# Kernel tuning notes

Hardware: AMD Instinct MI355X
Metric: run time of the kernel (lower is better)

## Reference

```python
import jax, jax.numpy as jnp
import numpy as np
from jax import lax


def _log_g(z):
    # log of g(x) = x + 0.5 if x >= 0 else sigmoid(x)
    return jnp.where(z >= 0, jnp.log(jax.nn.relu(z) + 0.5), -jax.nn.softplus(-z))


def setup_inputs() -> dict:
    key = jax.random.key(0)
    k1, k2, k3 = jax.random.split(key, 3)
    B, S, D, H = 8, 8192, 512, 256
    x = jax.random.normal(k1, (B, S, D), dtype=jnp.float32)
    h_prev = jax.random.normal(k2, (B, H), dtype=jnp.float32)
    # nn.Linear(D, 3H, bias=False) weight: [3H, D], scaled like torch default init
    W = jax.random.normal(k3, (3 * H, D), dtype=jnp.float32) * (1.0 / np.sqrt(D))
    return {"x": x, "h_prev": h_prev, "W": W}


def reference(x, h_prev, W):
    # x: [B,S,D], h_prev: [B,H], W: [3H,D]
    seq_len = x.shape[1]
    y = jnp.einsum("bsd,hd->bsh", x, W)              # [B,S,3H]
    f, i, h = jnp.split(y, 3, axis=-1)                # each [B,S,H]
    diff = jax.nn.softplus(-f) - jax.nn.softplus(-i)
    log_f = -jax.nn.softplus(diff)                    # log(sigmoid-normalized forget gate)
    log_i = -jax.nn.softplus(-diff)                   # log(input gate)
    log_h0 = _log_g(h_prev)                           # [B,H]
    log_tilde_h = _log_g(h)                           # [B,S,H]
    # parallel scan in log space: h_t = f_t * h_{t-1} + i_t * g(h_t~)
    a_star = jnp.concatenate(
        [jnp.zeros_like(log_h0)[:, None], jnp.cumsum(log_f, axis=1)], axis=1
    )                                                  # [B,S+1,H]
    log_vals = jnp.concatenate([log_h0[:, None], log_i + log_tilde_h], axis=1)  # [B,S+1,H]
    log_h = a_star + lax.cumlogsumexp(log_vals - a_star, axis=1)
    h_t = jnp.exp(log_h)                               # [B,S+1,H]
    return h_t[:, -seq_len:]                           # [B,S,H]
```

## Files before the change

kernel.cpp:

```cpp
#include <hip/hip_runtime.h>
#include <math.h>

#define BB 8
#define SS 8192
#define DD 512
#define HH 256
#define MM (BB * SS)
#define NN (3 * HH)
#define CC 64
#define LL 128

typedef unsigned short u16;
typedef __attribute__((ext_vector_type(8))) short short8;
typedef __attribute__((ext_vector_type(4))) float f32x4;

#define AS1(p) ((const __attribute__((address_space(1))) void*)(p))
#define AS3(p) ((__attribute__((address_space(3))) void*)(p))

__device__ __forceinline__ u16 f2bf(float f) {
    union { float f; unsigned u; } v; v.f = f;
    unsigned r = v.u + 0x7fffu + ((v.u >> 16) & 1u);
    return (u16)(r >> 16);
}

__device__ __forceinline__ float sp_fast(float z) {
    return (z > 15.0f) ? z : __logf(1.0f + __expf(z));
}

__global__ __launch_bounds__(256) void convert_x(const float4* __restrict__ x,
                                                 ushort4* __restrict__ xb, int n4) {
    int i = blockIdx.x * blockDim.x + threadIdx.x;
    const int stride = gridDim.x * blockDim.x;
    for (; i < n4; i += stride) {
        const float4 v = x[i];
        ushort4 o;
        o.x = f2bf(v.x); o.y = f2bf(v.y); o.z = f2bf(v.z); o.w = f2bf(v.w);
        xb[i] = o;
    }
}

__global__ __launch_bounds__(128) void convert_W(const float* __restrict__ W,
                                                 u16* __restrict__ Wr) {
    const int orow = blockIdx.x;
    const int hg = orow / 48, rem = orow % 48;
    const int g = rem >> 4, hl = rem & 15;
    const int irow = g * HH + hg * 16 + hl;
    const int t = threadIdx.x;
    const float4 v = *(const float4*)&W[(size_t)irow * DD + t * 4];
    ushort4 o;
    o.x = f2bf(v.x); o.y = f2bf(v.y); o.z = f2bf(v.z); o.w = f2bf(v.w);
    *(ushort4*)&Wr[(size_t)orow * DD + t * 4] = o;
}

__global__ __launch_bounds__(512) void gemm_gate_mfma(
    const u16* __restrict__ Wr,
    float* __restrict__ F_arr,
    void* xbuf)
{
    __shared__ __align__(16) u16 As[64 * 32];
    __shared__ __align__(16) u16 Bs[NN * 32];

    const u16* xb = (const u16*)xbuf;
    float* u_out = (float*)xbuf;

    const int tid = threadIdx.x;
    const int m0 = blockIdx.x * 64;
    const int w = tid >> 6;
    const int lane = tid & 63;
    const int l16 = lane & 15;
    const int quad = lane >> 4;

    f32x4 acc[4][6];
    #pragma unroll
    for (int a = 0; a < 4; ++a)
        #pragma unroll
        for (int b = 0; b < 6; ++b)
            #pragma unroll
            for (int e = 0; e < 4; ++e) acc[a][b][e] = 0.0f;

    for (int kit = 0; kit < DD / 32; ++kit) {
        const int k0 = kit * 32;
        __syncthreads();
        #pragma unroll
        for (int i = 0; i < 6; ++i) {
            const int idx = tid + 512 * i;
            const u16* g = Wr + ((size_t)(idx >> 2) * DD + k0 + (idx & 3) * 8);
            __builtin_amdgcn_global_load_lds(AS1(g), AS3(Bs + (size_t)idx * 8), 16, 0, 0);
        }
        if (tid < 256) {
            const int idx = tid;
            const u16* g = xb + ((size_t)(m0 + (idx >> 2)) * DD + k0 + (idx & 3) * 8);
            __builtin_amdgcn_global_load_lds(AS1(g), AS3(As + (size_t)idx * 8), 16, 0, 0);
        }
        __syncthreads();

        short8 a[4], b[6];
        #pragma unroll
        for (int mf = 0; mf < 4; ++mf)
            a[mf] = *(const short8*)&As[(mf * 16 + l16) * 32 + quad * 8];
        #pragma unroll
        for (int nf = 0; nf < 6; ++nf)
            b[nf] = *(const short8*)&Bs[(w * 96 + nf * 16 + l16) * 32 + quad * 8];
        #pragma unroll
        for (int mf = 0; mf < 4; ++mf)
            #pragma unroll
            for (int nf = 0; nf < 6; ++nf)
                acc[mf][nf] = __builtin_amdgcn_mfma_f32_16x16x32_bf16(
                    a[mf], b[nf], acc[mf][nf], 0, 0, 0);
    }

    #pragma unroll
    for (int mf = 0; mf < 4; ++mf) {
        #pragma unroll
        for (int hgl = 0; hgl < 2; ++hgl) {
            const int head = (2 * w + hgl) * 16 + l16;
            #pragma unroll
            for (int r = 0; r < 4; ++r) {
                const int m = m0 + mf * 16 + quad * 4 + r;
                const float fr = acc[mf][hgl * 3 + 0][r];
                const float ir = acc[mf][hgl * 3 + 1][r];
                const float hr = acc[mf][hgl * 3 + 2][r];
                const float diff = sp_fast(-fr) - sp_fast(-ir);
                const float F = __builtin_amdgcn_rcpf(1.0f + __expf(diff));
                const float I = 1.0f - F;
                const float G = (hr >= 0.0f) ? (hr + 0.5f)
                                             : __builtin_amdgcn_rcpf(1.0f + __expf(-hr));
                const size_t o = (size_t)m * HH + head;
                F_arr[o] = F;
                u_out[o] = I * G;
            }
        }
    }
}

__global__ __launch_bounds__(256) void scan_pass1(
    const float* __restrict__ F_arr, const float* __restrict__ u_arr,
    float* __restrict__ P_arr, float* __restrict__ U_arr) {
    const int bc = blockIdx.x;
    const int b = bc / CC;
    const int c = bc % CC;
    const int h = threadIdx.x;
    size_t base = ((size_t)(b * SS + c * LL)) * HH + h;
    float P = 1.0f, U = 0.0f;
    #pragma unroll 4
    for (int t = 0; t < LL; ++t) {
        const float F = F_arr[base];
        const float u = u_arr[base];
        U = F * U + u;
        P = P * F;
        base += HH;
    }
    const size_t o = ((size_t)c * BB + b) * HH + h;
    P_arr[o] = P;
    U_arr[o] = U;
}

__global__ __launch_bounds__(256) void scan_pass2(
    const float* __restrict__ h_prev, const float* __restrict__ P_arr,
    const float* __restrict__ U_arr, float* __restrict__ Hin) {
    const int b = blockIdx.x;
    const int h = threadIdx.x;
    const float z = h_prev[b * HH + h];
    float carry = (z >= 0.0f) ? (z + 0.5f) : __builtin_amdgcn_rcpf(1.0f + __expf(-z));
    for (int c = 0; c < CC; ++c) {
        const size_t o = ((size_t)c * BB + b) * HH + h;
        Hin[o] = carry;
        carry = P_arr[o] * carry + U_arr[o];
    }
}

__global__ __launch_bounds__(256) void scan_pass3(
    const float* __restrict__ F_arr, const float* __restrict__ Hin,
    float* __restrict__ out) {
    const int bc = blockIdx.x;
    const int b = bc / CC;
    const int c = bc % CC;
    const int h = threadIdx.x;
    float hv = Hin[((size_t)c * BB + b) * HH + h];
    size_t base = ((size_t)(b * SS + c * LL)) * HH + h;
    #pragma unroll 4
    for (int t = 0; t < LL; ++t) {
        const float F = F_arr[base];
        const float u = out[base];
        hv = F * hv + u;
        out[base] = hv;
        base += HH;
    }
}

extern "C" void kernel_launch(void* const* d_in, const int* in_sizes, int n_in,
                              void* d_out, int out_size, void* d_ws, size_t ws_size,
                              hipStream_t stream) {
    const float* x      = (const float*)d_in[0];
    const float* h_prev = (const float*)d_in[1];
    const float* W      = (const float*)d_in[2];

    float* F_arr = (float*)d_ws;
    float* P_arr = F_arr + (size_t)MM * HH;
    float* U_arr = P_arr + (size_t)CC * BB * HH;
    float* Hin   = U_arr + (size_t)CC * BB * HH;
    u16*   Wr    = (u16*)(Hin + (size_t)CC * BB * HH);

    convert_x<<<4096, 256, 0, stream>>>((const float4*)x, (ushort4*)d_out,
                                        (MM * DD) / 4);
    convert_W<<<NN, 128, 0, stream>>>(W, Wr);
    gemm_gate_mfma<<<MM / 64, 512, 0, stream>>>(Wr, F_arr, d_out);
    scan_pass1<<<BB * CC, HH, 0, stream>>>(F_arr, (const float*)d_out, P_arr, U_arr);
    scan_pass2<<<BB, HH, 0, stream>>>(h_prev, P_arr, U_arr, Hin);
    scan_pass3<<<BB * CC, HH, 0, stream>>>(F_arr, Hin, (float*)d_out);
}
```

Before: 387.9 us.

## Fuse x bf16 conversion into GEMM and double-buffer W tiles in LDS

Removes the separate convert_x pass: the GEMM now reads fp32 x directly, packs it to bf16 with round-to-nearest and stores it into a padded, double-buffered A tile in LDS. W is pre-packed into a tile-contiguous layout split into two N-halves, so each half is prefetched into LDS while the other is used by MFMA. The goal is to save a full read/write pass over x (about 128MB in, 64MB out) and to overlap loads with compute. In exchange the GEMM reads twice as many A bytes, rounding of x changes slightly, and the kernel uses more LDS per block, which may lower occupancy.

Measured after the change: 346.8 us. 1.12x faster.

```diff
diff --git a/kernel.cpp b/kernel.cpp
--- a/kernel.cpp
+++ b/kernel.cpp
@@ -6,7 +6,7 @@
 #define DD 512
 #define HH 256
 #define MM (BB * SS)
-#define NN (3 * HH)
+#define NN 768
 #define CC 64
 #define LL 128
 
@@ -17,51 +17,48 @@
 #define AS1(p) ((const __attribute__((address_space(1))) void*)(p))
 #define AS3(p) ((__attribute__((address_space(3))) void*)(p))
 
-__device__ __forceinline__ u16 f2bf(float f) {
+__device__ __forceinline__ u16 f2bf_rtne(float f) {
     union { float f; unsigned u; } v; v.f = f;
     unsigned r = v.u + 0x7fffu + ((v.u >> 16) & 1u);
     return (u16)(r >> 16);
 }
+__device__ __forceinline__ unsigned pack2_rtn(float a, float b) {
+    union { float f; unsigned u; } x, y; x.f = a; y.f = b;
+    return ((x.u + 0x8000u) >> 16) | ((y.u + 0x8000u) & 0xffff0000u);
+}
 
 __device__ __forceinline__ float sp_fast(float z) {
     return (z > 15.0f) ? z : __logf(1.0f + __expf(z));
 }
 
-__global__ __launch_bounds__(256) void convert_x(const float4* __restrict__ x,
-                                                 ushort4* __restrict__ xb, int n4) {
-    int i = blockIdx.x * blockDim.x + threadIdx.x;
-    const int stride = gridDim.x * blockDim.x;
-    for (; i < n4; i += stride) {
-        const float4 v = x[i];
-        ushort4 o;
-        o.x = f2bf(v.x); o.y = f2bf(v.y); o.z = f2bf(v.z); o.w = f2bf(v.w);
-        xb[i] = o;
-    }
-}
-
-__global__ __launch_bounds__(128) void convert_W(const float* __restrict__ W,
+__global__ __launch_bounds__(256) void convert_W(const float* __restrict__ W,
                                                  u16* __restrict__ Wr) {
-    const int orow = blockIdx.x;
-    const int hg = orow / 48, rem = orow % 48;
-    const int g = rem >> 4, hl = rem & 15;
-    const int irow = g * HH + hg * 16 + hl;
-    const int t = threadIdx.x;
-    const float4 v = *(const float4*)&W[(size_t)irow * DD + t * 4];
-    ushort4 o;
-    o.x = f2bf(v.x); o.y = f2bf(v.y); o.z = f2bf(v.z); o.w = f2bf(v.w);
-    *(ushort4*)&Wr[(size_t)orow * DD + t * 4] = o;
+    const int chunk = blockIdx.x * 256 + threadIdx.x;
+    const int kh = chunk / 1536;
+    const int rem = chunk % 1536;
+    const int cl = rem >> 2, qq = rem & 3;
+    const int kc = kh >> 1, half = kh & 1;
+    const int c = half * 384 + cl;
+    const int hg = c / 48, r48 = c % 48;
+    const int g = r48 >> 4, hl = r48 & 15;
+    const int wrow = g * HH + hg * 16 + hl;
+    const int k0 = kc * 32 + qq * 8;
+    const float4 v0 = *(const float4*)&W[(size_t)wrow * DD + k0];
+    const float4 v1 = *(const float4*)&W[(size_t)wrow * DD + k0 + 4];
+    u16 o[8];
+    o[0]=f2bf_rtne(v0.x); o[1]=f2bf_rtne(v0.y); o[2]=f2bf_rtne(v0.z); o[3]=f2bf_rtne(v0.w);
+    o[4]=f2bf_rtne(v1.x); o[5]=f2bf_rtne(v1.y); o[6]=f2bf_rtne(v1.z); o[7]=f2bf_rtne(v1.w);
+    *(uint4*)&Wr[(size_t)chunk * 8] = *(const uint4*)o;
 }
 
 __global__ __launch_bounds__(512) void gemm_gate_mfma(
+    const float* __restrict__ x,
     const u16* __restrict__ Wr,
     float* __restrict__ F_arr,
-    void* xbuf)
+    float* __restrict__ u_out)
 {
-    __shared__ __align__(16) u16 As[64 * 32];
-    __shared__ __align__(16) u16 Bs[NN * 32];
-
-    const u16* xb = (const u16*)xbuf;
-    float* u_out = (float*)xbuf;
+    __shared__ __align__(16) u16 Bs[2][12288];
+    __shared__ __align__(16) u16 As[2][64 * 40];
 
     const int tid = threadIdx.x;
     const int m0 = blockIdx.x * 64;
@@ -70,6 +67,9 @@
     const int l16 = lane & 15;
     const int quad = lane >> 4;
 
+    const int arow = tid >> 3;
+    const int aqi = tid & 7;
+
     f32x4 acc[4][6];
     #pragma unroll
     for (int a = 0; a < 4; ++a)
@@ -78,48 +78,90 @@
             #pragma unroll
             for (int e = 0; e < 4; ++e) acc[a][b][e] = 0.0f;
 
-    for (int kit = 0; kit < DD / 32; ++kit) {
-        const int k0 = kit * 32;
-        __syncthreads();
-        #pragma unroll
-        for (int i = 0; i < 6; ++i) {
-            const int idx = tid + 512 * i;
-            const u16* g = Wr + ((size_t)(idx >> 2) * DD + k0 + (idx & 3) * 8);
-            __builtin_amdgcn_global_load_lds(AS1(g), AS3(Bs + (size_t)idx * 8), 16, 0, 0);
-        }
-        if (tid < 256) {
-            const int idx = tid;
-            const u16* g = xb + ((size_t)(m0 + (idx >> 2)) * DD + k0 + (idx & 3) * 8);
-            __builtin_amdgcn_global_load_lds(AS1(g), AS3(As + (size_t)idx * 8), 16, 0, 0);
-        }
-        __syncthreads();
-
-        short8 a[4], b[6];
+    #pragma unroll
+    for (int i = 0; i < 3; ++i) {
+        const int idx = i * 512 + tid;
+        __builtin_amdgcn_global_load_lds(AS1(Wr + (size_t)idx * 8),
+                                         AS3(&Bs[0][idx * 8]), 16, 0, 0);
+    }
+    {
+        const float4 v = *(const float4*)&x[(size_t)(m0 + arow) * DD + aqi * 4];
+        *(uint2*)&As[0][arow * 40 + aqi * 4] =
+            make_uint2(pack2_rtn(v.x, v.y), pack2_rtn(v.z, v.w));
+    }
+    float4 a_reg = *(const float4*)&x[(size_t)(m0 + arow) * DD + 32 + aqi * 4];
+    __syncthreads();
+
+    for (int kc = 0; kc < 16; ++kc) {
+        {
+            const size_t base = ((size_t)(kc * 2 + 1)) * 12288;
+            #pragma unroll
+            for (int i = 0; i < 3; ++i) {
+                const int idx = i * 512 + tid;
+                __builtin_amdgcn_global_load_lds(AS1(Wr + base + (size_t)idx * 8),
+                                                 AS3(&Bs[1][idx * 8]), 16, 0, 0);
+            }
+        }
+        short8 afr[4];
         #pragma unroll
         for (int mf = 0; mf < 4; ++mf)
-            a[mf] = *(const short8*)&As[(mf * 16 + l16) * 32 + quad * 8];
+            afr[mf] = *(const short8*)&As[kc & 1][(mf * 16 + l16) * 40 + quad * 8];
+
+        {
+            short8 bfr[3];
+            #pragma unroll
+            for (int jn = 0; jn < 3; ++jn)
+                bfr[jn] = *(const short8*)&Bs[0][((w * 3 + jn) * 16 + l16) * 32 + quad * 8];
+            #pragma unroll
+            for (int mf = 0; mf < 4; ++mf)
+                #pragma unroll
+                for (int jn = 0; jn < 3; ++jn)
+                    acc[mf][jn] = __builtin_amdgcn_mfma_f32_16x16x32_bf16(
+                        afr[mf], bfr[jn], acc[mf][jn], 0, 0, 0);
+        }
+        *(uint2*)&As[(kc + 1) & 1][arow * 40 + aqi * 4] =
+            make_uint2(pack2_rtn(a_reg.x, a_reg.y), pack2_rtn(a_reg.z, a_reg.w));
+        {
+            const int knext = (kc + 2 < 16) ? (kc + 2) : 15;
+            a_reg = *(const float4*)&x[(size_t)(m0 + arow) * DD + knext * 32 + aqi * 4];
+        }
+        __syncthreads();
+
+        if (kc < 15) {
+            const size_t base = ((size_t)((kc + 1) * 2)) * 12288;
+            #pragma unroll
+            for (int i = 0; i < 3; ++i) {
+                const int idx = i * 512 + tid;
+                __builtin_amdgcn_global_load_lds(AS1(Wr + base + (size_t)idx * 8),
+                                                 AS3(&Bs[0][idx * 8]), 16, 0, 0);
+            }
+        }
+        {
+            short8 bfr[3];
+            #pragma unroll
+            for (int jn = 0; jn < 3; ++jn)
+                bfr[jn] = *(const short8*)&Bs[1][((w * 3 + jn) * 16 + l16) * 32 + quad * 8];
+            #pragma unroll
+            for (int mf = 0; mf < 4; ++mf)
+                #pragma unroll
+                for (int jn = 0; jn < 3; ++jn)
+                    acc[mf][3 + jn] = __builtin_amdgcn_mfma_f32_16x16x32_bf16(
+                        afr[mf], bfr[jn], acc[mf][3 + jn], 0, 0, 0);
+        }
+        __syncthreads();
+    }
+
+    #pragma unroll
+    for (int half = 0; half < 2; ++half) {
+        const int head = (half * 8 + w) * 16 + l16;
         #pragma unroll
-        for (int nf = 0; nf < 6; ++nf)
-            b[nf] = *(const short8*)&Bs[(w * 96 + nf * 16 + l16) * 32 + quad * 8];
-        #pragma unroll
-        for (int mf = 0; mf < 4; ++mf)
-            #pragma unroll
-            for (int nf = 0; nf < 6; ++nf)
-                acc[mf][nf] = __builtin_amdgcn_mfma_f32_16x16x32_bf16(
-                    a[mf], b[nf], acc[mf][nf], 0, 0, 0);
-    }
-
-    #pragma unroll
-    for (int mf = 0; mf < 4; ++mf) {
-        #pragma unroll
-        for (int hgl = 0; hgl < 2; ++hgl) {
-            const int head = (2 * w + hgl) * 16 + l16;
+        for (int mf = 0; mf < 4; ++mf) {
             #pragma unroll
             for (int r = 0; r < 4; ++r) {
                 const int m = m0 + mf * 16 + quad * 4 + r;
-                const float fr = acc[mf][hgl * 3 + 0][r];
-                const float ir = acc[mf][hgl * 3 + 1][r];
-                const float hr = acc[mf][hgl * 3 + 2][r];
+                const float fr = acc[mf][half * 3 + 0][r];
+                const float ir = acc[mf][half * 3 + 1][r];
+                const float hr = acc[mf][half * 3 + 2][r];
                 const float diff = sp_fast(-fr) - sp_fast(-ir);
                 const float F = __builtin_amdgcn_rcpf(1.0f + __expf(diff));
                 const float I = 1.0f - F;
@@ -201,10 +243,8 @@
     float* Hin   = U_arr + (size_t)CC * BB * HH;
     u16*   Wr    = (u16*)(Hin + (size_t)CC * BB * HH);
 
-    convert_x<<<4096, 256, 0, stream>>>((const float4*)x, (ushort4*)d_out,
-                                        (MM * DD) / 4);
-    convert_W<<<NN, 128, 0, stream>>>(W, Wr);
-    gemm_gate_mfma<<<MM / 64, 512, 0, stream>>>(Wr, F_arr, d_out);
+    convert_W<<<192, 256, 0, stream>>>(W, Wr);
+    gemm_gate_mfma<<<MM / 64, 512, 0, stream>>>(x, Wr, F_arr, (float*)d_out);
     scan_pass1<<<BB * CC, HH, 0, stream>>>(F_arr, (const float*)d_out, P_arr, U_arr);
     scan_pass2<<<BB, HH, 0, stream>>>(h_prev, P_arr, U_arr, Hin);
     scan_pass3<<<BB * CC, HH, 0, stream>>>(F_arr, Hin, (float*)d_out);
```

## Fuse x conversion and chunk scan into GEMM epilogue, pack F/u as bf16

Applied to the files above, without the earlier changes.

Drops the separate x-to-bf16 kernel: the GEMM now reads fp32 x directly into registers, converts it, and feeds MFMA from registers with software prefetch instead of LDS staging. The GEMM epilogue also computes per-64-row chunk products and sums via wave shuffles, which removes the first scan pass. F and u are stored as a packed bf16 pair to halve intermediate traffic. The cost is lower precision in the recurrence inputs (round-to-nearest bf16 for F, u, P and U), which may hurt accuracy over long chains, and each wave now loads its A and B operands from global memory without LDS sharing.

Result: slower. 429.8 us (+10.8%).

```diff
diff --git a/kernel.cpp b/kernel.cpp
--- a/kernel.cpp
+++ b/kernel.cpp
@@ -6,37 +6,28 @@
 #define DD 512
 #define HH 256
 #define MM (BB * SS)
-#define NN (3 * HH)
 #define CC 64
 #define LL 128
 
 typedef unsigned short u16;
+typedef unsigned int u32;
 typedef __attribute__((ext_vector_type(8))) short short8;
 typedef __attribute__((ext_vector_type(4))) float f32x4;
 
-#define AS1(p) ((const __attribute__((address_space(1))) void*)(p))
-#define AS3(p) ((__attribute__((address_space(3))) void*)(p))
-
-__device__ __forceinline__ u16 f2bf(float f) {
+__device__ __forceinline__ u16 f2bf_rtne(float f) {
     union { float f; unsigned u; } v; v.f = f;
     unsigned r = v.u + 0x7fffu + ((v.u >> 16) & 1u);
     return (u16)(r >> 16);
 }
+__device__ __forceinline__ u32 pack2_rtn(float a, float b) {
+    union { float f; unsigned u; } x, y; x.f = a; y.f = b;
+    return ((x.u + 0x8000u) >> 16) | ((y.u + 0x8000u) & 0xffff0000u);
+}
+__device__ __forceinline__ float bf_lo(u32 w) { return __uint_as_float(w << 16); }
+__device__ __forceinline__ float bf_hi(u32 w) { return __uint_as_float(w & 0xffff0000u); }
 
 __device__ __forceinline__ float sp_fast(float z) {
     return (z > 15.0f) ? z : __logf(1.0f + __expf(z));
-}
-
-__global__ __launch_bounds__(256) void convert_x(const float4* __restrict__ x,
-                                                 ushort4* __restrict__ xb, int n4) {
-    int i = blockIdx.x * blockDim.x + threadIdx.x;
-    const int stride = gridDim.x * blockDim.x;
-    for (; i < n4; i += stride) {
-        const float4 v = x[i];
-        ushort4 o;
-        o.x = f2bf(v.x); o.y = f2bf(v.y); o.z = f2bf(v.z); o.w = f2bf(v.w);
-        xb[i] = o;
-    }
 }
 
 __global__ __launch_bounds__(128) void convert_W(const float* __restrict__ W,
@@ -48,27 +39,25 @@
     const int t = threadIdx.x;
     const float4 v = *(const float4*)&W[(size_t)irow * DD + t * 4];
     ushort4 o;
-    o.x = f2bf(v.x); o.y = f2bf(v.y); o.z = f2bf(v.z); o.w = f2bf(v.w);
+    o.x = f2bf_rtne(v.x); o.y = f2bf_rtne(v.y); o.z = f2bf_rtne(v.z); o.w = f2bf_rtne(v.w);
     *(ushort4*)&Wr[(size_t)orow * DD + t * 4] = o;
 }
 
-__global__ __launch_bounds__(512) void gemm_gate_mfma(
+__global__ __launch_bounds__(512, 2) void gemm_gate_scan(
+    const float* __restrict__ x,
     const u16* __restrict__ Wr,
-    float* __restrict__ F_arr,
-    void* xbuf)
+    u32* __restrict__ FU,
+    u32* __restrict__ PU)
 {
-    __shared__ __align__(16) u16 As[64 * 32];
-    __shared__ __align__(16) u16 Bs[NN * 32];
-
-    const u16* xb = (const u16*)xbuf;
-    float* u_out = (float*)xbuf;
-
     const int tid = threadIdx.x;
-    const int m0 = blockIdx.x * 64;
     const int w = tid >> 6;
     const int lane = tid & 63;
     const int l16 = lane & 15;
     const int quad = lane >> 4;
+    const int m0 = blockIdx.x * 64;
+
+    const float* xp = x + (size_t)(m0 + l16) * DD + quad * 8;
+    const u16* wp = Wr + (size_t)(w * 96 + l16) * DD + quad * 8;
 
     f32x4 acc[4][6];
     #pragma unroll
@@ -78,99 +67,126 @@
             #pragma unroll
             for (int e = 0; e < 4; ++e) acc[a][b][e] = 0.0f;
 
-    for (int kit = 0; kit < DD / 32; ++kit) {
-        const int k0 = kit * 32;
-        __syncthreads();
-        #pragma unroll
-        for (int i = 0; i < 6; ++i) {
-            const int idx = tid + 512 * i;
-            const u16* g = Wr + ((size_t)(idx >> 2) * DD + k0 + (idx & 3) * 8);
-            __builtin_amdgcn_global_load_lds(AS1(g), AS3(Bs + (size_t)idx * 8), 16, 0, 0);
-        }
-        if (tid < 256) {
-            const int idx = tid;
-            const u16* g = xb + ((size_t)(m0 + (idx >> 2)) * DD + k0 + (idx & 3) * 8);
-            __builtin_amdgcn_global_load_lds(AS1(g), AS3(As + (size_t)idx * 8), 16, 0, 0);
-        }
-        __syncthreads();
-
-        short8 a[4], b[6];
-        #pragma unroll
-        for (int mf = 0; mf < 4; ++mf)
-            a[mf] = *(const short8*)&As[(mf * 16 + l16) * 32 + quad * 8];
-        #pragma unroll
-        for (int nf = 0; nf < 6; ++nf)
-            b[nf] = *(const short8*)&Bs[(w * 96 + nf * 16 + l16) * 32 + quad * 8];
+    short8 ca[4], cb[6];
+    #pragma unroll
+    for (int mf = 0; mf < 4; ++mf) {
+        const float4 v0 = *(const float4*)(xp + (size_t)mf * 16 * DD);
+        const float4 v1 = *(const float4*)(xp + (size_t)mf * 16 * DD + 4);
+        u32 q[4] = { pack2_rtn(v0.x, v0.y), pack2_rtn(v0.z, v0.w),
+                     pack2_rtn(v1.x, v1.y), pack2_rtn(v1.z, v1.w) };
+        ca[mf] = *(const short8*)q;
+    }
+    #pragma unroll
+    for (int nf = 0; nf < 6; ++nf)
+        cb[nf] = *(const short8*)(wp + (size_t)nf * 16 * DD);
+
+    #pragma unroll
+    for (int ks = 0; ks < 16; ++ks) {
+        short8 na[4], nb[6];
+        if (ks < 15) {
+            const int ko = (ks + 1) * 32;
+            #pragma unroll
+            for (int mf = 0; mf < 4; ++mf) {
+                const float4 v0 = *(const float4*)(xp + (size_t)mf * 16 * DD + ko);
+                const float4 v1 = *(const float4*)(xp + (size_t)mf * 16 * DD + ko + 4);
+                u32 q[4] = { pack2_rtn(v0.x, v0.y), pack2_rtn(v0.z, v0.w),
+                             pack2_rtn(v1.x, v1.y), pack2_rtn(v1.z, v1.w) };
+                na[mf] = *(const short8*)q;
+            }
+            #pragma unroll
+            for (int nf = 0; nf < 6; ++nf)
+                nb[nf] = *(const short8*)(wp + (size_t)nf * 16 * DD + ko);
+        }
         #pragma unroll
         for (int mf = 0; mf < 4; ++mf)
             #pragma unroll
             for (int nf = 0; nf < 6; ++nf)
                 acc[mf][nf] = __builtin_amdgcn_mfma_f32_16x16x32_bf16(
-                    a[mf], b[nf], acc[mf][nf], 0, 0, 0);
-    }
+                    ca[mf], cb[nf], acc[mf][nf], 0, 0, 0);
+        if (ks < 15) {
+            #pragma unroll
+            for (int mf = 0; mf < 4; ++mf) ca[mf] = na[mf];
+            #pragma unroll
+            for (int nf = 0; nf < 6; ++nf) cb[nf] = nb[nf];
+        }
+    }
+
+    float Pg[2], Ug[2];
+    #pragma unroll
+    for (int hg = 0; hg < 2; ++hg) { Pg[hg] = 1.0f; Ug[hg] = 0.0f; }
 
     #pragma unroll
     for (int mf = 0; mf < 4; ++mf) {
-        #pragma unroll
-        for (int hgl = 0; hgl < 2; ++hgl) {
-            const int head = (2 * w + hgl) * 16 + l16;
-            #pragma unroll
-            for (int r = 0; r < 4; ++r) {
-                const int m = m0 + mf * 16 + quad * 4 + r;
-                const float fr = acc[mf][hgl * 3 + 0][r];
-                const float ir = acc[mf][hgl * 3 + 1][r];
-                const float hr = acc[mf][hgl * 3 + 2][r];
+        float P[2] = {1.0f, 1.0f}, U[2] = {0.0f, 0.0f};
+        #pragma unroll
+        for (int r = 0; r < 4; ++r) {
+            const int m = m0 + mf * 16 + quad * 4 + r;
+            #pragma unroll
+            for (int hg = 0; hg < 2; ++hg) {
+                const float fr = acc[mf][hg * 3 + 0][r];
+                const float ir = acc[mf][hg * 3 + 1][r];
+                const float hr = acc[mf][hg * 3 + 2][r];
                 const float diff = sp_fast(-fr) - sp_fast(-ir);
                 const float F = __builtin_amdgcn_rcpf(1.0f + __expf(diff));
                 const float I = 1.0f - F;
                 const float G = (hr >= 0.0f) ? (hr + 0.5f)
                                              : __builtin_amdgcn_rcpf(1.0f + __expf(-hr));
-                const size_t o = (size_t)m * HH + head;
-                F_arr[o] = F;
-                u_out[o] = I * G;
+                const float u = I * G;
+                FU[(size_t)m * HH + (2 * w + hg) * 16 + l16] = pack2_rtn(F, u);
+                U[hg] = U[hg] * F + u;
+                P[hg] = P[hg] * F;
             }
         }
-    }
-}
-
-__global__ __launch_bounds__(256) void scan_pass1(
-    const float* __restrict__ F_arr, const float* __restrict__ u_arr,
-    float* __restrict__ P_arr, float* __restrict__ U_arr) {
-    const int bc = blockIdx.x;
-    const int b = bc / CC;
-    const int c = bc % CC;
-    const int h = threadIdx.x;
-    size_t base = ((size_t)(b * SS + c * LL)) * HH + h;
-    float P = 1.0f, U = 0.0f;
-    #pragma unroll 4
-    for (int t = 0; t < LL; ++t) {
-        const float F = F_arr[base];
-        const float u = u_arr[base];
-        U = F * U + u;
-        P = P * F;
-        base += HH;
-    }
-    const size_t o = ((size_t)c * BB + b) * HH + h;
-    P_arr[o] = P;
-    U_arr[o] = U;
+        #pragma unroll
+        for (int s = 0; s < 2; ++s) {
+            const int mask = 16 << s;
+            const bool late = (s == 0) ? (quad & 1) : ((quad >> 1) & 1);
+            #pragma unroll
+            for (int hg = 0; hg < 2; ++hg) {
+                const float oP = __shfl_xor(P[hg], mask, 64);
+                const float oU = __shfl_xor(U[hg], mask, 64);
+                const float eP = late ? oP : P[hg];
+                const float eU = late ? oU : U[hg];
+                const float lP = late ? P[hg] : oP;
+                const float lU = late ? U[hg] : oU;
+                P[hg] = eP * lP;
+                U[hg] = eU * lP + lU;
+            }
+        }
+        #pragma unroll
+        for (int hg = 0; hg < 2; ++hg) {
+            Ug[hg] = Ug[hg] * P[hg] + U[hg];
+            Pg[hg] = Pg[hg] * P[hg];
+        }
+    }
+    if (lane < 16) {
+        const int b = m0 >> 13;
+        const int grp = (m0 & 8191) >> 6;
+        #pragma unroll
+        for (int hg = 0; hg < 2; ++hg)
+            PU[((size_t)b * 128 + grp) * HH + (2 * w + hg) * 16 + l16] =
+                pack2_rtn(Pg[hg], Ug[hg]);
+    }
 }
 
 __global__ __launch_bounds__(256) void scan_pass2(
-    const float* __restrict__ h_prev, const float* __restrict__ P_arr,
-    const float* __restrict__ U_arr, float* __restrict__ Hin) {
+    const float* __restrict__ h_prev, const u32* __restrict__ PU,
+    float* __restrict__ Hin) {
     const int b = blockIdx.x;
     const int h = threadIdx.x;
     const float z = h_prev[b * HH + h];
     float carry = (z >= 0.0f) ? (z + 0.5f) : __builtin_amdgcn_rcpf(1.0f + __expf(-z));
-    for (int c = 0; c < CC; ++c) {
-        const size_t o = ((size_t)c * BB + b) * HH + h;
-        Hin[o] = carry;
-        carry = P_arr[o] * carry + U_arr[o];
+    #pragma unroll 8
+    for (int grp = 0; grp < 128; ++grp) {
+        if ((grp & 1) == 0)
+            Hin[((size_t)(grp >> 1) * BB + b) * HH + h] = carry;
+        const u32 pu = PU[((size_t)b * 128 + grp) * HH + h];
+        carry = bf_lo(pu) * carry + bf_hi(pu);
     }
 }
 
 __global__ __launch_bounds__(256) void scan_pass3(
-    const float* __restrict__ F_arr, const float* __restrict__ Hin,
+    const u32* __restrict__ FU, const float* __restrict__ Hin,
     float* __restrict__ out) {
     const int bc = blockIdx.x;
     const int b = bc / CC;
@@ -180,9 +196,8 @@
     size_t base = ((size_t)(b * SS + c * LL)) * HH + h;
     #pragma unroll 4
     for (int t = 0; t < LL; ++t) {
-        const float F = F_arr[base];
-        const float u = out[base];
-        hv = F * hv + u;
+        const u32 fu = FU[base];
+        hv = bf_lo(fu) * hv + bf_hi(fu);
         out[base] = hv;
         base += HH;
     }
@@ -195,17 +210,13 @@
     const float* h_prev = (const float*)d_in[1];
     const float* W      = (const float*)d_in[2];
 
-    float* F_arr = (float*)d_ws;
-    float* P_arr = F_arr + (size_t)MM * HH;
-    float* U_arr = P_arr + (size_t)CC * BB * HH;
-    float* Hin   = U_arr + (size_t)CC * BB * HH;
-    u16*   Wr    = (u16*)(Hin + (size_t)CC * BB * HH);
-
-    convert_x<<<4096, 256, 0, stream>>>((const float4*)x, (ushort4*)d_out,
-                                        (MM * DD) / 4);
-    convert_W<<<NN, 128, 0, stream>>>(W, Wr);
-    gemm_gate_mfma<<<MM / 64, 512, 0, stream>>>(Wr, F_arr, d_out);
-    scan_pass1<<<BB * CC, HH, 0, stream>>>(F_arr, (const float*)d_out, P_arr, U_arr);
-    scan_pass2<<<BB, HH, 0, stream>>>(h_prev, P_arr, U_arr, Hin);
-    scan_pass3<<<BB * CC, HH, 0, stream>>>(F_arr, Hin, (float*)d_out);
-}
+    u32*   FU  = (u32*)d_ws;
+    float* Hin = (float*)(FU + (size_t)MM * HH);
+    u16*   Wr  = (u16*)(Hin + (size_t)CC * BB * HH);
+    u32*   PU  = (u32*)d_out;
+
+    convert_W<<<768, 128, 0, stream>>>(W, Wr);
+    gemm_gate_scan<<<MM / 64, 512, 0, stream>>>(x, Wr, FU, PU);
+    scan_pass2<<<BB, HH, 0, stream>>>(h_prev, PU, Hin);
+    scan_pass3<<<BB * CC, HH, 0, stream>>>(FU, Hin, (float*)d_out);
+}
```
